# Kernel optimization log

Hardware: AMD Instinct MI355X
Metric: run time of the kernel (lower is better)

## Reference

```python
import jax, jax.numpy as jnp
import numpy as np

N_HEAD = 12

def setup_inputs() -> dict:
    key = jax.random.key(0)
    k1, k2, k3 = jax.random.split(key, 3)
    nx = 768
    B, S = 2, 2048
    return {
        "hidden_states": jax.random.normal(k1, (B, S, nx), dtype=jnp.float32),
        "w_attn": jax.random.normal(k2, (nx, 3 * nx), dtype=jnp.float32) * 0.02,
        "b_attn": jnp.zeros((3 * nx,), dtype=jnp.float32),
        "w_proj": jax.random.normal(k3, (nx, nx), dtype=jnp.float32) * 0.02,
        "b_proj": jnp.zeros((nx,), dtype=jnp.float32),
    }

def reference(hidden_states, w_attn, b_attn, w_proj, b_proj):
    B, S, nx = hidden_states.shape
    d_head = nx // N_HEAD
    qkv = hidden_states @ w_attn + b_attn  # [B,S,3nx]
    q, k, v = jnp.split(qkv, 3, axis=-1)
    # split heads -> [B,H,S,d]
    def split(x):
        return x.reshape(B, S, N_HEAD, d_head).transpose(0, 2, 1, 3)
    q, k, v = split(q), split(k), split(v)
    # scale=True: divide by sqrt(d_head) (v.size(-1))
    w = jnp.einsum("bhsd,bhtd->bhst", q, k) / jnp.sqrt(jnp.float32(d_head))
    w = jax.nn.softmax(w, axis=-1)
    a = jnp.einsum("bhst,bhtd->bhsd", w, v)  # [B,H,S,d]
    a = a.transpose(0, 2, 1, 3).reshape(B, S, nx)  # merge heads
    return a @ w_proj + b_proj
```

## Files before the change

kernel.cpp:

```cpp
#include <hip/hip_runtime.h>

#define NHEAD 12
#define DHEAD 64
#define SEQ   2048
#define NB    2
#define NX    768
#define MTOK  (NB * SEQ)

typedef __attribute__((ext_vector_type(8))) short short8;
typedef __attribute__((ext_vector_type(4))) short short4v;
typedef __attribute__((ext_vector_type(4))) float f32x4;

__device__ __forceinline__ unsigned short f2bf(float x) {
    union { float f; unsigned u; } v; v.f = x;
    unsigned r = v.u + 0x7fffu + ((v.u >> 16) & 1u);
    return (unsigned short)(r >> 16);
}

__device__ __forceinline__ unsigned pkbf(float a, float b) {
    unsigned r;
    asm("v_cvt_pk_bf16_f32 %0, %1, %2" : "=v"(r) : "v"(a), "v"(b));
    return r;
}

__device__ __forceinline__ float fexp2(float x) {
#if __has_builtin(__builtin_amdgcn_exp2f)
    return __builtin_amdgcn_exp2f(x);
#else
    float r; asm("v_exp_f32 %0, %1" : "=v"(r) : "v"(x)); return r;
#endif
}

#define MFMA32(a, b, c) __builtin_amdgcn_mfma_f32_16x16x32_bf16(a, b, c, 0, 0, 0)

__global__ __launch_bounds__(256)
void cvt_all(const float* __restrict__ hs,
             const float* __restrict__ wa, const float* __restrict__ wp,
             unsigned short* __restrict__ Abf,
             unsigned short* __restrict__ WtA, unsigned short* __restrict__ WtP)
{
    __shared__ float tile[32][33];
    const int bid = blockIdx.x;
    const int t = threadIdx.x;

    if (bid < 3072) {
        int i = bid * 256 + t;
        if (i >= 786432) return;
        float4 v = ((const float4*)hs)[i];
        union { ushort4 v4; unsigned u[2]; } o;
        o.u[0] = pkbf(v.x, v.y);
        o.u[1] = pkbf(v.z, v.w);
        ((ushort4*)Abf)[i] = o.v4;
        return;
    }

    const float* W; unsigned short* T; int K, N, bx, by;
    if (bid < 4800) {
        int b2 = bid - 3072;
        bx = b2 % 72; by = b2 / 72;
        W = wa; T = WtA; K = NX; N = 3 * NX;
    } else {
        int b2 = bid - 4800;
        bx = b2 % 24; by = b2 / 24;
        W = wp; T = WtP; K = NX; N = NX;
    }
    const int r = t >> 5, c = t & 31;
    const int k0 = by * 32, n0 = bx * 32;
#pragma unroll
    for (int i = 0; i < 4; i++)
        tile[r + i * 8][c] = W[(size_t)(k0 + r + i * 8) * N + n0 + c];
    __syncthreads();
#pragma unroll
    for (int i = 0; i < 4; i++) {
        int n = r + i * 8;
        T[(size_t)(n0 + n) * K + k0 + c] = f2bf(tile[c][n]);
    }
}

template<int MODE>
__global__ __launch_bounds__(256, 3)
void gemm_bf(const unsigned short* __restrict__ A,
             const unsigned short* __restrict__ Bt,
             const float* __restrict__ bias,
             float* __restrict__ fo,
             unsigned short* __restrict__ qb, unsigned short* __restrict__ kb2,
             unsigned short* __restrict__ vtb,
             int M, int N, int K)
{
    __shared__ __align__(16) unsigned char sm[2][16384];
    const int t = threadIdx.x;
    const int w = t >> 6, lane = t & 63;
    const int lo16 = lane & 15, quad = lane >> 4;

    const int nwg  = gridDim.x * gridDim.y;
    const int flat = blockIdx.y * gridDim.x + blockIdx.x;
    const int swz  = (flat & 7) * (nwg >> 3) + (flat >> 3);
    const int ib = (swz / gridDim.x) * 128, jb = (swz % gridDim.x) * 128;

    f32x4 acc[4][4];
#pragma unroll
    for (int mt = 0; mt < 4; mt++)
#pragma unroll
        for (int nt = 0; nt < 4; nt++) acc[mt][nt] = (f32x4){0.f, 0.f, 0.f, 0.f};

    const int srow = lane >> 2;
    const int sj   = lane & 3;

    auto stage = [&](int buf, int k0) {
#pragma unroll
        for (int i = 0; i < 4; i++) {
            const int u   = i * 4 + w;
            const int p   = u >> 3;
            const int row = (u & 7) * 16 + srow;
            const int sc  = sj ^ (row & 3);
            const unsigned short* g = (p == 0)
                ? (A  + (size_t)(ib + row) * K + k0 + sc * 8)
                : (Bt + (size_t)(jb + row) * K + k0 + sc * 8);
            void* lp = &sm[buf][p * 8192 + (u & 7) * 1024];
            __builtin_amdgcn_global_load_lds(
                (const __attribute__((address_space(1))) unsigned int*)g,
                (__attribute__((address_space(3))) unsigned int*)lp, 16, 0, 0);
        }
    };

    const int mrow = (w >> 1) * 64;
    const int nrow = (w & 1) * 64;

    stage(0, 0);
    const int NIT = K / 32;
    for (int kt = 0; kt < NIT; kt++) {
        const int buf = kt & 1;
        __syncthreads();
        if (kt + 1 < NIT) stage(buf ^ 1, (kt + 1) * 32);

        short8 af[4], bf[4];
#pragma unroll
        for (int mt = 0; mt < 4; mt++) {
            const int row = mrow + mt * 16 + lo16;
            af[mt] = *(const short8*)&sm[buf][row * 64 + ((quad ^ (row & 3)) * 16)];
        }
#pragma unroll
        for (int nt = 0; nt < 4; nt++) {
            const int row = nrow + nt * 16 + lo16;
            bf[nt] = *(const short8*)&sm[buf][8192 + row * 64 + ((quad ^ (row & 3)) * 16)];
        }
#pragma unroll
        for (int mt = 0; mt < 4; mt++)
#pragma unroll
            for (int nt = 0; nt < 4; nt++)
                acc[mt][nt] = MFMA32(af[mt], bf[nt], acc[mt][nt]);
    }

    if constexpr (MODE == 0) {
        const int which = jb / NX;
#pragma unroll
        for (int nt = 0; nt < 4; nt++) {
            const int j  = jb + nrow + nt * 16 + lo16;
            const int cc = j - which * NX;
            const int hh = cc >> 6, dd = cc & 63;
            const float bj = bias[j];
#pragma unroll
            for (int mt = 0; mt < 4; mt++) {
                const int m0 = ib + mrow + mt * 16 + quad * 4;
                const int bb = m0 >> 11;
                const int s0 = m0 & 2047;
                const size_t hb = (size_t)(bb * NHEAD + hh);
                if (which == 2) {
                    union { ushort4 v4; unsigned u[2]; } pv;
                    pv.u[0] = pkbf(acc[mt][nt][0] + bj, acc[mt][nt][1] + bj);
                    pv.u[1] = pkbf(acc[mt][nt][2] + bj, acc[mt][nt][3] + bj);
                    *(ushort4*)(vtb + (hb * DHEAD + dd) * SEQ + s0) = pv.v4;
                } else {
                    unsigned short* dst = (which == 0) ? qb : kb2;
                    const float sc = (which == 0) ? 0.18033688011112042f : 1.0f;
#pragma unroll
                    for (int r = 0; r < 4; r++)
                        dst[(hb * SEQ + s0 + r) * DHEAD + dd] =
                            f2bf((acc[mt][nt][r] + bj) * sc);
                }
            }
        }
    } else {
#pragma unroll
        for (int nt = 0; nt < 4; nt++) {
            const int j  = jb + nrow + nt * 16 + lo16;
            const float bj = bias[j];
#pragma unroll
            for (int mt = 0; mt < 4; mt++) {
                const int m0 = ib + mrow + mt * 16 + quad * 4;
#pragma unroll
                for (int r = 0; r < 4; r++)
                    fo[(size_t)(m0 + r) * N + j] = acc[mt][nt][r] + bj;
            }
        }
    }
}

__global__ __launch_bounds__(256, 3)
void attn_bf(const unsigned short* __restrict__ qb, const unsigned short* __restrict__ kb,
             const unsigned short* __restrict__ vtb, unsigned short* __restrict__ ab)
{
    __shared__ __align__(16) unsigned char sm[2][16384];
    const int t = threadIdx.x;
    const int w = t >> 6, lane = t & 63;
    const int lo16 = lane & 15, quad = lane >> 4;

    const int id = blockIdx.x;
    const int xcd = id & 7, slot = id >> 3;
    const int bh = xcd * 3 + slot % 3;
    const int q0 = (slot / 3) * 64;
    const int b = bh / NHEAD, h = bh % NHEAD;

    const unsigned short* Qb = qb  + (size_t)bh * SEQ * DHEAD;
    const unsigned short* Kb = kb  + (size_t)bh * SEQ * DHEAD;
    const unsigned short* Vb = vtb + (size_t)bh * DHEAD * SEQ;

    short8 qf[2];
    {
        const size_t qo = (size_t)(q0 + w * 16 + lo16) * DHEAD + quad * 8;
        qf[0] = *(const short8*)(Qb + qo);
        qf[1] = *(const short8*)(Qb + qo + 32);
    }

    const short8 ones = (short8){0x3F80, 0x3F80, 0x3F80, 0x3F80,
                                 0x3F80, 0x3F80, 0x3F80, 0x3F80};

    const int srow = lane >> 3;
    const int sj   = lane & 7;
    auto stage = [&](int buf, int k0) {
#pragma unroll
        for (int i = 0; i < 4; i++) {
            const int u   = i * 4 + w;
            const int p   = u >> 3;
            const int row = (u & 7) * 8 + srow;
            const int sc  = sj ^ (row & 7);
            const int gr  = (row & 32) | (((row >> 2) & 3) << 3)
                          | (((row >> 4) & 1) << 2) | (row & 3);
            const unsigned short* g = (p == 0)
                ? (Kb + (size_t)(k0 + gr) * DHEAD + sc * 8)
                : (Vb + (size_t)row * SEQ + k0 + sc * 8);
            void* lp = &sm[buf][p * 8192 + (u & 7) * 1024];
            __builtin_amdgcn_global_load_lds(
                (const __attribute__((address_space(1))) unsigned int*)g,
                (__attribute__((address_space(3))) unsigned int*)lp, 16, 0, 0);
        }
    };

    f32x4 oacc[4];
#pragma unroll
    for (int dt = 0; dt < 4; dt++) oacc[dt] = (f32x4){0.f, 0.f, 0.f, 0.f};
    f32x4 lacc = (f32x4){0.f, 0.f, 0.f, 0.f};

    stage(0, 0);
    for (int kt = 0; kt < SEQ / 64; kt++) {
        const int buf = kt & 1;
        __syncthreads();
        if (kt + 1 < SEQ / 64) stage(buf ^ 1, (kt + 1) * 64);

        f32x4 s[4];
#pragma unroll
        for (int rt = 0; rt < 4; rt++) {
            const int row = rt * 16 + lo16;
            const int rs = row & 7;
            short8 kf0 = *(const short8*)&sm[buf][row * 128 + ((quad ^ rs) * 16)];
            short8 kf1 = *(const short8*)&sm[buf][row * 128 + (((4 + quad) ^ rs) * 16)];
            f32x4 a = (f32x4){0.f, 0.f, 0.f, 0.f};
            a = MFMA32(kf0, qf[0], a);
            a = MFMA32(kf1, qf[1], a);
            s[rt] = a;
        }

        short8 pf[2];
#pragma unroll
        for (int f = 0; f < 2; f++) {
            float e0 = fexp2(s[2 * f][0]),     e1 = fexp2(s[2 * f][1]);
            float e2 = fexp2(s[2 * f][2]),     e3 = fexp2(s[2 * f][3]);
            float e4 = fexp2(s[2 * f + 1][0]), e5 = fexp2(s[2 * f + 1][1]);
            float e6 = fexp2(s[2 * f + 1][2]), e7 = fexp2(s[2 * f + 1][3]);
            union { short8 s8; unsigned u[4]; } pk;
            pk.u[0] = pkbf(e0, e1);
            pk.u[1] = pkbf(e2, e3);
            pk.u[2] = pkbf(e4, e5);
            pk.u[3] = pkbf(e6, e7);
            pf[f] = pk.s8;
        }

        __builtin_amdgcn_s_setprio(1);
        lacc = MFMA32(ones, pf[0], lacc);
        lacc = MFMA32(ones, pf[1], lacc);
#pragma unroll
        for (int dt = 0; dt < 4; dt++) {
            const int row = dt * 16 + lo16;
            const int rs = row & 7;
            short8 vf0 = *(const short8*)&sm[buf][8192 + row * 128 + ((quad ^ rs) * 16)];
            short8 vf1 = *(const short8*)&sm[buf][8192 + row * 128 + (((4 + quad) ^ rs) * 16)];
            f32x4 a = oacc[dt];
            a = MFMA32(vf0, pf[0], a);
            a = MFMA32(vf1, pf[1], a);
            oacc[dt] = a;
        }
        __builtin_amdgcn_s_setprio(0);
    }

    const float inv = 1.0f / lacc[0];

    unsigned short* dst = ab + (size_t)(b * SEQ + q0 + w * 16 + lo16) * NX + h * DHEAD;
#pragma unroll
    for (int dt = 0; dt < 4; dt++) {
        union { ushort4 v4; unsigned u[2]; } pv;
        pv.u[0] = pkbf(oacc[dt][0] * inv, oacc[dt][1] * inv);
        pv.u[1] = pkbf(oacc[dt][2] * inv, oacc[dt][3] * inv);
        *(ushort4*)(dst + dt * 16 + quad * 4) = pv.v4;
    }
}

extern "C" void kernel_launch(void* const* d_in, const int* in_sizes, int n_in,
                              void* d_out, int out_size, void* d_ws, size_t ws_size,
                              hipStream_t stream)
{
    const float* hs     = (const float*)d_in[0];
    const float* w_attn = (const float*)d_in[1];
    const float* b_attn = (const float*)d_in[2];
    const float* w_proj = (const float*)d_in[3];
    const float* b_proj = (const float*)d_in[4];
    float* out = (float*)d_out;

    unsigned short* wsu = (unsigned short*)d_ws;
    unsigned short* Abf  = wsu;
    unsigned short* WtA  = Abf  + 3145728;
    unsigned short* WtP  = WtA  + 1769472;
    unsigned short* qbuf = WtP  + 589824;
    unsigned short* kbuf = qbuf + 3145728;
    unsigned short* vtbf = kbuf + 3145728;
    unsigned short* abf  = vtbf + 3145728;

    cvt_all<<<5376, 256, 0, stream>>>(hs, w_attn, w_proj, Abf, WtA, WtP);

    gemm_bf<0><<<dim3(18, 32), 256, 0, stream>>>(
        Abf, WtA, b_attn, nullptr, qbuf, kbuf, vtbf, MTOK, 3 * NX, NX);

    attn_bf<<<768, 256, 0, stream>>>(qbuf, kbuf, vtbf, abf);

    gemm_bf<1><<<dim3(6, 32), 256, 0, stream>>>(
        abf, WtP, b_proj, out, nullptr, nullptr, nullptr, MTOK, NX, NX);
}
```

Measured before the change: 150.8 us.

## Split attention key tiles across waves instead of query rows, reduce partials in LDS

The attention kernel now has each wave own a 16-key slice of every 64-key tile for all 64 queries, instead of 16 queries over all keys. Each wave accumulates partial P·V outputs with 16x16x16 MFMAs and computes row sums in scalar code instead of using a ones-matrix MFMA. The four waves then merge their partials through LDS with a tree reduction. This trades four times the output accumulator registers and an end-of-kernel LDS reduction with extra barriers for fewer K fragment reads per wave. The extra register pressure may lower occupancy below the declared launch bounds.

```diff
diff --git a/kernel.cpp b/kernel.cpp
--- a/kernel.cpp
+++ b/kernel.cpp
@@ -32,6 +32,7 @@
 }
 
 #define MFMA32(a, b, c) __builtin_amdgcn_mfma_f32_16x16x32_bf16(a, b, c, 0, 0, 0)
+#define MFMA16(a, b, c) __builtin_amdgcn_mfma_f32_16x16x16bf16_1k(a, b, c, 0, 0, 0)
 
 __global__ __launch_bounds__(256)
 void cvt_all(const float* __restrict__ hs,
@@ -201,6 +202,7 @@
              const unsigned short* __restrict__ vtb, unsigned short* __restrict__ ab)
 {
     __shared__ __align__(16) unsigned char sm[2][16384];
+    __shared__ float lsw[256];
     const int t = threadIdx.x;
     const int w = t >> 6, lane = t & 63;
     const int lo16 = lane & 15, quad = lane >> 4;
@@ -215,15 +217,13 @@
     const unsigned short* Kb = kb  + (size_t)bh * SEQ * DHEAD;
     const unsigned short* Vb = vtb + (size_t)bh * DHEAD * SEQ;
 
-    short8 qf[2];
-    {
-        const size_t qo = (size_t)(q0 + w * 16 + lo16) * DHEAD + quad * 8;
-        qf[0] = *(const short8*)(Qb + qo);
-        qf[1] = *(const short8*)(Qb + qo + 32);
-    }
-
-    const short8 ones = (short8){0x3F80, 0x3F80, 0x3F80, 0x3F80,
-                                 0x3F80, 0x3F80, 0x3F80, 0x3F80};
+    short8 qf[4][2];
+#pragma unroll
+    for (int qt = 0; qt < 4; qt++) {
+        const size_t qo = (size_t)(q0 + qt * 16 + lo16) * DHEAD + quad * 8;
+        qf[qt][0] = *(const short8*)(Qb + qo);
+        qf[qt][1] = *(const short8*)(Qb + qo + 32);
+    }
 
     const int srow = lane >> 3;
     const int sj   = lane & 7;
@@ -234,10 +234,8 @@
             const int p   = u >> 3;
             const int row = (u & 7) * 8 + srow;
             const int sc  = sj ^ (row & 7);
-            const int gr  = (row & 32) | (((row >> 2) & 3) << 3)
-                          | (((row >> 4) & 1) << 2) | (row & 3);
             const unsigned short* g = (p == 0)
-                ? (Kb + (size_t)(k0 + gr) * DHEAD + sc * 8)
+                ? (Kb + (size_t)(k0 + row) * DHEAD + sc * 8)
                 : (Vb + (size_t)row * SEQ + k0 + sc * 8);
             void* lp = &sm[buf][p * 8192 + (u & 7) * 1024];
             __builtin_amdgcn_global_load_lds(
@@ -246,10 +244,15 @@
         }
     };
 
-    f32x4 oacc[4];
-#pragma unroll
-    for (int dt = 0; dt < 4; dt++) oacc[dt] = (f32x4){0.f, 0.f, 0.f, 0.f};
-    f32x4 lacc = (f32x4){0.f, 0.f, 0.f, 0.f};
+    f32x4 oacc[4][4];
+#pragma unroll
+    for (int qt = 0; qt < 4; qt++)
+#pragma unroll
+        for (int dt = 0; dt < 4; dt++) oacc[qt][dt] = (f32x4){0.f, 0.f, 0.f, 0.f};
+    float lsum[4] = {0.f, 0.f, 0.f, 0.f};
+
+    const int krow = w * 16 + lo16;
+    const int krs  = krow & 7;
 
     stage(0, 0);
     for (int kt = 0; kt < SEQ / 64; kt++) {
@@ -257,60 +260,100 @@
         __syncthreads();
         if (kt + 1 < SEQ / 64) stage(buf ^ 1, (kt + 1) * 64);
 
+        short8 kf0 = *(const short8*)&sm[buf][krow * 128 + ((quad ^ krs) * 16)];
+        short8 kf1 = *(const short8*)&sm[buf][krow * 128 + (((4 + quad) ^ krs) * 16)];
+
         f32x4 s[4];
 #pragma unroll
-        for (int rt = 0; rt < 4; rt++) {
-            const int row = rt * 16 + lo16;
-            const int rs = row & 7;
-            short8 kf0 = *(const short8*)&sm[buf][row * 128 + ((quad ^ rs) * 16)];
-            short8 kf1 = *(const short8*)&sm[buf][row * 128 + (((4 + quad) ^ rs) * 16)];
+        for (int qt = 0; qt < 4; qt++) {
             f32x4 a = (f32x4){0.f, 0.f, 0.f, 0.f};
-            a = MFMA32(kf0, qf[0], a);
-            a = MFMA32(kf1, qf[1], a);
-            s[rt] = a;
-        }
-
-        short8 pf[2];
-#pragma unroll
-        for (int f = 0; f < 2; f++) {
-            float e0 = fexp2(s[2 * f][0]),     e1 = fexp2(s[2 * f][1]);
-            float e2 = fexp2(s[2 * f][2]),     e3 = fexp2(s[2 * f][3]);
-            float e4 = fexp2(s[2 * f + 1][0]), e5 = fexp2(s[2 * f + 1][1]);
-            float e6 = fexp2(s[2 * f + 1][2]), e7 = fexp2(s[2 * f + 1][3]);
-            union { short8 s8; unsigned u[4]; } pk;
+            a = MFMA32(kf0, qf[qt][0], a);
+            a = MFMA32(kf1, qf[qt][1], a);
+            s[qt] = a;
+        }
+
+        short4v pf[4];
+#pragma unroll
+        for (int qt = 0; qt < 4; qt++) {
+            float e0 = fexp2(s[qt][0]), e1 = fexp2(s[qt][1]);
+            float e2 = fexp2(s[qt][2]), e3 = fexp2(s[qt][3]);
+            lsum[qt] += (e0 + e1) + (e2 + e3);
+            union { short4v s4; unsigned u[2]; } pk;
             pk.u[0] = pkbf(e0, e1);
             pk.u[1] = pkbf(e2, e3);
-            pk.u[2] = pkbf(e4, e5);
-            pk.u[3] = pkbf(e6, e7);
-            pf[f] = pk.s8;
+            pf[qt] = pk.s4;
         }
 
         __builtin_amdgcn_s_setprio(1);
-        lacc = MFMA32(ones, pf[0], lacc);
-        lacc = MFMA32(ones, pf[1], lacc);
 #pragma unroll
         for (int dt = 0; dt < 4; dt++) {
             const int row = dt * 16 + lo16;
             const int rs = row & 7;
-            short8 vf0 = *(const short8*)&sm[buf][8192 + row * 128 + ((quad ^ rs) * 16)];
-            short8 vf1 = *(const short8*)&sm[buf][8192 + row * 128 + (((4 + quad) ^ rs) * 16)];
-            f32x4 a = oacc[dt];
-            a = MFMA32(vf0, pf[0], a);
-            a = MFMA32(vf1, pf[1], a);
-            oacc[dt] = a;
+            const int ch = (2 * w + (quad >> 1)) ^ rs;
+            short4v vf = *(const short4v*)&sm[buf][8192 + row * 128 + ch * 16 + (quad & 1) * 8];
+#pragma unroll
+            for (int qt = 0; qt < 4; qt++)
+                oacc[qt][dt] = MFMA16(vf, pf[qt], oacc[qt][dt]);
         }
         __builtin_amdgcn_s_setprio(0);
     }
 
-    const float inv = 1.0f / lacc[0];
-
-    unsigned short* dst = ab + (size_t)(b * SEQ + q0 + w * 16 + lo16) * NX + h * DHEAD;
-#pragma unroll
-    for (int dt = 0; dt < 4; dt++) {
-        union { ushort4 v4; unsigned u[2]; } pv;
-        pv.u[0] = pkbf(oacc[dt][0] * inv, oacc[dt][1] * inv);
-        pv.u[1] = pkbf(oacc[dt][2] * inv, oacc[dt][3] * inv);
-        *(ushort4*)(dst + dt * 16 + quad * 4) = pv.v4;
+#pragma unroll
+    for (int qt = 0; qt < 4; qt++) {
+        lsum[qt] += __shfl_xor(lsum[qt], 16);
+        lsum[qt] += __shfl_xor(lsum[qt], 32);
+    }
+    if (quad == 0)
+#pragma unroll
+        for (int qt = 0; qt < 4; qt++) lsw[w * 64 + qt * 16 + lo16] = lsum[qt];
+
+    float* fs = (float*)sm;
+    __syncthreads();
+    if (w & 1) {
+        const int reg = (w >> 1) * 4096;
+#pragma unroll
+        for (int qt = 0; qt < 4; qt++)
+#pragma unroll
+            for (int dt = 0; dt < 4; dt++)
+                *(f32x4*)&fs[reg + ((qt * 4 + dt) * 64 + lane) * 4] = oacc[qt][dt];
+    }
+    __syncthreads();
+    if (w == 0 || w == 2) {
+        const int reg = (w >> 1) * 4096;
+#pragma unroll
+        for (int qt = 0; qt < 4; qt++)
+#pragma unroll
+            for (int dt = 0; dt < 4; dt++)
+                oacc[qt][dt] += *(const f32x4*)&fs[reg + ((qt * 4 + dt) * 64 + lane) * 4];
+    }
+    __syncthreads();
+    if (w == 2) {
+#pragma unroll
+        for (int qt = 0; qt < 4; qt++)
+#pragma unroll
+            for (int dt = 0; dt < 4; dt++)
+                *(f32x4*)&fs[((qt * 4 + dt) * 64 + lane) * 4] = oacc[qt][dt];
+    }
+    __syncthreads();
+    if (w == 0) {
+#pragma unroll
+        for (int qt = 0; qt < 4; qt++) {
+#pragma unroll
+            for (int dt = 0; dt < 4; dt++)
+                oacc[qt][dt] += *(const f32x4*)&fs[((qt * 4 + dt) * 64 + lane) * 4];
+            const float tot = lsw[qt * 16 + lo16]       + lsw[64 + qt * 16 + lo16]
+                            + lsw[128 + qt * 16 + lo16] + lsw[192 + qt * 16 + lo16];
+            const float inv = 1.0f / tot;
+            unsigned short* dst =
+                ab + (size_t)(b * SEQ + q0 + qt * 16 + lo16) * NX + h * DHEAD;
+#pragma unroll
+            for (int dt = 0; dt < 4; dt++) {
+                union { ushort4 v4; unsigned u[2]; } pv;
+                pv.u[0] = pkbf(oacc[qt][dt][0] * inv, oacc[qt][dt][1] * inv);
+                pv.u[1] = pkbf(oacc[qt][dt][2] * inv, oacc[qt][dt][3] * inv);
+                *(ushort4*)(dst + dt * 16 + quad * 4) = pv.v4;
+            }
+        }
     }
 }
 
```

New measurement: 154.1 us. +2.2%, slower.

## Double attention KV tile to 128 keys and compute row sums in VALU

Applied to the files above, without the earlier changes.

The attention kernel now stages 128 keys per iteration instead of 64, doubling shared memory per buffer and halving the number of barrier-separated iterations. Launch bounds drop from 3 to 2 blocks per CU to match the larger LDS footprint. The softmax denominator is now accumulated as fp32 sums of the exponentials plus cross-lane shuffles, replacing the extra MFMA against a ones vector. This trades occupancy for fewer syncs and fewer matrix instructions, and it raises register pressure from the larger score tile.

```diff
diff --git a/kernel.cpp b/kernel.cpp
--- a/kernel.cpp
+++ b/kernel.cpp
@@ -196,11 +196,11 @@
     }
 }
 
-__global__ __launch_bounds__(256, 3)
+__global__ __launch_bounds__(256, 2)
 void attn_bf(const unsigned short* __restrict__ qb, const unsigned short* __restrict__ kb,
              const unsigned short* __restrict__ vtb, unsigned short* __restrict__ ab)
 {
-    __shared__ __align__(16) unsigned char sm[2][16384];
+    __shared__ __align__(16) unsigned char sm[2][32768];
     const int t = threadIdx.x;
     const int w = t >> 6, lane = t & 63;
     const int lo16 = lane & 15, quad = lane >> 4;
@@ -222,24 +222,24 @@
         qf[1] = *(const short8*)(Qb + qo + 32);
     }
 
-    const short8 ones = (short8){0x3F80, 0x3F80, 0x3F80, 0x3F80,
-                                 0x3F80, 0x3F80, 0x3F80, 0x3F80};
-
     const int srow = lane >> 3;
     const int sj   = lane & 7;
     auto stage = [&](int buf, int k0) {
 #pragma unroll
-        for (int i = 0; i < 4; i++) {
+        for (int i = 0; i < 8; i++) {
             const int u   = i * 4 + w;
-            const int p   = u >> 3;
+            const int sub = u >> 3;
             const int row = (u & 7) * 8 + srow;
             const int sc  = sj ^ (row & 7);
-            const int gr  = (row & 32) | (((row >> 2) & 3) << 3)
-                          | (((row >> 4) & 1) << 2) | (row & 3);
-            const unsigned short* g = (p == 0)
-                ? (Kb + (size_t)(k0 + gr) * DHEAD + sc * 8)
-                : (Vb + (size_t)row * SEQ + k0 + sc * 8);
-            void* lp = &sm[buf][p * 8192 + (u & 7) * 1024];
+            const unsigned short* g;
+            if (sub < 2) {
+                const int gr = (row & 32) | (((row >> 2) & 3) << 3)
+                             | (((row >> 4) & 1) << 2) | (row & 3);
+                g = Kb + (size_t)(k0 + sub * 64 + gr) * DHEAD + sc * 8;
+            } else {
+                g = Vb + (size_t)row * SEQ + k0 + (sub - 2) * 64 + sc * 8;
+            }
+            void* lp = &sm[buf][u * 1024];
             __builtin_amdgcn_global_load_lds(
                 (const __attribute__((address_space(1))) unsigned int*)g,
                 (__attribute__((address_space(3))) unsigned int*)lp, 16, 0, 0);
@@ -249,60 +249,66 @@
     f32x4 oacc[4];
 #pragma unroll
     for (int dt = 0; dt < 4; dt++) oacc[dt] = (f32x4){0.f, 0.f, 0.f, 0.f};
-    f32x4 lacc = (f32x4){0.f, 0.f, 0.f, 0.f};
+    float lsum = 0.f;
 
     stage(0, 0);
-    for (int kt = 0; kt < SEQ / 64; kt++) {
+    for (int kt = 0; kt < SEQ / 128; kt++) {
         const int buf = kt & 1;
         __syncthreads();
-        if (kt + 1 < SEQ / 64) stage(buf ^ 1, (kt + 1) * 64);
-
-        f32x4 s[4];
-#pragma unroll
-        for (int rt = 0; rt < 4; rt++) {
-            const int row = rt * 16 + lo16;
-            const int rs = row & 7;
-            short8 kf0 = *(const short8*)&sm[buf][row * 128 + ((quad ^ rs) * 16)];
-            short8 kf1 = *(const short8*)&sm[buf][row * 128 + (((4 + quad) ^ rs) * 16)];
+        if (kt + 1 < SEQ / 128) stage(buf ^ 1, (kt + 1) * 128);
+
+        f32x4 s[8];
+#pragma unroll
+        for (int rt = 0; rt < 8; rt++) {
+            const int base = (rt >> 2) * 8192;
+            const int row  = (rt & 3) * 16 + lo16;
+            const int rs   = row & 7;
+            short8 kf0 = *(const short8*)&sm[buf][base + row * 128 + ((quad ^ rs) * 16)];
+            short8 kf1 = *(const short8*)&sm[buf][base + row * 128 + (((4 + quad) ^ rs) * 16)];
             f32x4 a = (f32x4){0.f, 0.f, 0.f, 0.f};
             a = MFMA32(kf0, qf[0], a);
             a = MFMA32(kf1, qf[1], a);
             s[rt] = a;
         }
 
-        short8 pf[2];
-#pragma unroll
-        for (int f = 0; f < 2; f++) {
-            float e0 = fexp2(s[2 * f][0]),     e1 = fexp2(s[2 * f][1]);
-            float e2 = fexp2(s[2 * f][2]),     e3 = fexp2(s[2 * f][3]);
-            float e4 = fexp2(s[2 * f + 1][0]), e5 = fexp2(s[2 * f + 1][1]);
-            float e6 = fexp2(s[2 * f + 1][2]), e7 = fexp2(s[2 * f + 1][3]);
+        short8 pf[4];
+#pragma unroll
+        for (int g = 0; g < 4; g++) {
+            float e0 = fexp2(s[2 * g][0]),     e1 = fexp2(s[2 * g][1]);
+            float e2 = fexp2(s[2 * g][2]),     e3 = fexp2(s[2 * g][3]);
+            float e4 = fexp2(s[2 * g + 1][0]), e5 = fexp2(s[2 * g + 1][1]);
+            float e6 = fexp2(s[2 * g + 1][2]), e7 = fexp2(s[2 * g + 1][3]);
+            lsum += ((e0 + e1) + (e2 + e3)) + ((e4 + e5) + (e6 + e7));
             union { short8 s8; unsigned u[4]; } pk;
             pk.u[0] = pkbf(e0, e1);
             pk.u[1] = pkbf(e2, e3);
             pk.u[2] = pkbf(e4, e5);
             pk.u[3] = pkbf(e6, e7);
-            pf[f] = pk.s8;
+            pf[g] = pk.s8;
         }
 
         __builtin_amdgcn_s_setprio(1);
-        lacc = MFMA32(ones, pf[0], lacc);
-        lacc = MFMA32(ones, pf[1], lacc);
 #pragma unroll
         for (int dt = 0; dt < 4; dt++) {
             const int row = dt * 16 + lo16;
             const int rs = row & 7;
-            short8 vf0 = *(const short8*)&sm[buf][8192 + row * 128 + ((quad ^ rs) * 16)];
-            short8 vf1 = *(const short8*)&sm[buf][8192 + row * 128 + (((4 + quad) ^ rs) * 16)];
             f32x4 a = oacc[dt];
-            a = MFMA32(vf0, pf[0], a);
-            a = MFMA32(vf1, pf[1], a);
+#pragma unroll
+            for (int hh2 = 0; hh2 < 2; hh2++) {
+                const int vbase = 16384 + hh2 * 8192;
+                short8 vf0 = *(const short8*)&sm[buf][vbase + row * 128 + ((quad ^ rs) * 16)];
+                short8 vf1 = *(const short8*)&sm[buf][vbase + row * 128 + (((4 + quad) ^ rs) * 16)];
+                a = MFMA32(vf0, pf[2 * hh2], a);
+                a = MFMA32(vf1, pf[2 * hh2 + 1], a);
+            }
             oacc[dt] = a;
         }
         __builtin_amdgcn_s_setprio(0);
     }
 
-    const float inv = 1.0f / lacc[0];
+    lsum += __shfl_xor(lsum, 16);
+    lsum += __shfl_xor(lsum, 32);
+    const float inv = 1.0f / lsum;
 
     unsigned short* dst = ab + (size_t)(b * SEQ + q0 + w * 16 + lo16) * NX + h * DHEAD;
 #pragma unroll
```

Measured after the change: 154.3 us. +2.3%, slower.
